# Optimization experiments

Measured on AMD Instinct MI355X. Metric: run time of the kernel, lower is better.

The kernel has to match this reference:

```python
import jax, jax.numpy as jnp
import numpy as np

BLANK = 0
SIZE_AVERAGE = True


def rnnt_loss(acts, labels, act_lens, label_lens):
    # acts: (B, T, U+1, V) raw logits; warp-transducer applies log_softmax internally
    B, T, U1, V = acts.shape
    U = U1 - 1
    logp = jax.nn.log_softmax(acts, axis=-1)          # (B,T,U1,V)
    lp_blank = logp[..., BLANK]                       # (B,T,U1)
    # emission log-prob of label u at grid point (t,u): logp[b,t,u,labels[b,u]]
    lp_emit = jnp.take_along_axis(
        logp[:, :, :U, :], labels[:, None, :, None].astype(jnp.int32), axis=3
    )[..., 0]                                         # (B,T,U)

    # alpha[0,0]=0 ; alpha[0,u] = sum_{k<u} emit[0,k]
    row0 = jnp.concatenate(
        [jnp.zeros((B, 1), acts.dtype), jnp.cumsum(lp_emit[:, 0, :], axis=1)], axis=1
    )                                                 # (B,U1)

    def outer(prev_row, xs):
        blank_prev, emit_t = xs                       # (B,U1), (B,U)
        fb = prev_row + blank_prev                    # arrive via blank from t-1
        def inner(carry, x):
            fb_u, em_prev = x                         # (B,), (B,)
            a = jnp.logaddexp(fb_u, carry + em_prev)  # blank vs emit path
            return a, a
        _, rest = jax.lax.scan(inner, fb[:, 0], (fb[:, 1:].T, emit_t.T))  # (U,B)
        row = jnp.concatenate([fb[:, :1], rest.T], axis=1)               # (B,U1)
        return row, row

    xs = (jnp.moveaxis(lp_blank[:, :-1, :], 1, 0),   # (T-1,B,U1)
          jnp.moveaxis(lp_emit[:, 1:, :], 1, 0))     # (T-1,B,U)
    _, rows = jax.lax.scan(outer, row0, xs)          # (T-1,B,U1)
    alpha = jnp.concatenate([row0[None], rows], axis=0)  # (T,B,U1)

    b_idx = jnp.arange(B)
    t_idx = act_lens.astype(jnp.int32) - 1
    u_idx = label_lens.astype(jnp.int32)
    loglike = alpha[t_idx, b_idx, u_idx] + lp_blank[b_idx, t_idx, u_idx]
    total = -jnp.sum(loglike)
    if SIZE_AVERAGE:
        total = total / B
    return total.reshape(1)


def setup_inputs() -> dict:
    key = jax.random.key(0)
    k1, k2, k3, k4 = jax.random.split(key, 4)
    B, T, U, V = 8, 256, 100, 128
    acts = jax.random.normal(k1, (B, T, U + 1, V), dtype=jnp.float32)
    labels = jax.random.randint(k2, (B, U), 0, V, dtype=jnp.int64)
    act_lens = jax.random.randint(k3, (B,), T // 2, T + 1, dtype=jnp.int32)
    label_lens = jax.random.randint(k4, (B,), U // 2, U + 1, dtype=jnp.int32)
    return {"acts": acts, "labels": labels, "act_lens": act_lens, "label_lens": label_lens}


def reference(acts, labels, act_lens, label_lens):
    return rnnt_loss(acts, labels, act_lens, label_lens)
```

## Files before the change

### kernel.cpp

```cpp
#include <hip/hip_runtime.h>
#include <math.h>

#define B_DIM  8
#define T_DIM  256
#define U_DIM  100
#define U1_DIM 101
#define V_DIM  128

#define ROWU   128
#define DROWS  360
#define NEGF   (-8.0e29f)
#define LOG2E  1.4426950408889634f
#define LN2    0.69314718055994530942f

#define VROWU  312
#define NITMAX 88
#define LDS_BYTES (NITMAX * VROWU * 4)

typedef unsigned uv2 __attribute__((ext_vector_type(2)));

__device__ __forceinline__ float ubit(unsigned u) { return __builtin_bit_cast(float, u); }

__device__ __forceinline__ float logadd2(float a, float b) {
    float m = fmaxf(a, b);
    float e = exp2f(-fabsf(a - b));
    return m + log2f(1.0f + e);
}
__device__ __forceinline__ float lse3(float a, float b, float c) {
    float m = fmaxf(fmaxf(a, b), c);
    float s = exp2f(a - m) + exp2f(b - m) + exp2f(c - m);
    return m + log2f(s);
}
__device__ __forceinline__ float lse5(float a, float b, float c, float d, float e) {
    float m = fmaxf(fmaxf(fmaxf(a, b), c), fmaxf(d, e));
    float s = exp2f(a - m) + exp2f(b - m) + exp2f(c - m) + exp2f(d - m) + exp2f(e - m);
    return m + log2f(s);
}

__device__ __forceinline__ float lane_shr1(float x) {
    int r = __builtin_amdgcn_update_dpp(0, __builtin_bit_cast(int, x),
                                        0x138 , 0xF, 0xF, true);
    return __builtin_bit_cast(float, r);
}

__device__ __forceinline__ unsigned f2bf(float f) {
    unsigned u = __builtin_bit_cast(unsigned, f);
    u += 0x7FFF + ((u >> 16) & 1);
    return u >> 16;
}

__global__ __launch_bounds__(256) void lsm_kernel(
    const float* __restrict__ acts, const int* __restrict__ labels,
    const int* __restrict__ act_lens, const int* __restrict__ label_lens,
    unsigned short* __restrict__ comb, int* __restrict__ counter, int nrows)
{
    if (blockIdx.x == 0 && threadIdx.x == 0) *counter = 0;

    int rid = blockIdx.x * 8 + (threadIdx.x >> 5);
    if (rid >= nrows) return;
    int hl = threadIdx.x & 31;

    int u  = rid % U1_DIM;
    int bt = rid / U1_DIM;
    int b  = bt / T_DIM;
    int t  = bt - b * T_DIM;
    if (t >= act_lens[b] || u > label_lens[b]) return;

    const float* row = acts + (size_t)rid * V_DIM;
    float4 x = *reinterpret_cast<const float4*>(row + 4 * hl);
    float4 y = make_float4(x.x * LOG2E, x.y * LOG2E, x.z * LOG2E, x.w * LOG2E);

    float s = exp2f(y.x) + exp2f(y.y) + exp2f(y.z) + exp2f(y.w);
    #pragma unroll
    for (int off = 16; off; off >>= 1) s += __shfl_xor(s, off);
    float lse2 = log2f(s);

    unsigned short* C = comb + (size_t)b * DROWS * (ROWU * 2);
    int d = t + u + 1;

    if (hl == 0)
        C[(size_t)d * (ROWU * 2) + 2 * u] = (unsigned short)f2bf(y.x - lse2);
    if (u < U_DIM) {
        int lab = labels[b * U_DIM + u];
        if (hl == (lab >> 2)) {
            int r = lab & 3;
            float v = (r == 0) ? y.x : (r == 1) ? y.y : (r == 2) ? y.z : y.w;
            C[(size_t)d * (ROWU * 2) + 2 * u + 3] = (unsigned short)f2bf(v - lse2);
        }
    }
}

struct W2 { float tA, mA, lA, tB, mB, lB; };
__device__ __forceinline__ W2 buildW2m(uv2 c0, uv2 cm, int l, int d, int tl, int ul) {
    const int ua = 2 * l, ub = 2 * l + 1;
    float BL0a = ubit(c0.x << 16), EM0a = ubit(c0.x & 0xFFFF0000u);
    float BL0b = ubit(c0.y << 16), EM0b = ubit(c0.y & 0xFFFF0000u);
    float BLma = ubit(cm.x << 16), EMma = ubit(cm.x & 0xFFFF0000u);
    float BLmb = ubit(cm.y << 16), EMmb = ubit(cm.y & 0xFFFF0000u);
    BL0a = (ua <= ul && (unsigned)(d - 1 - ua) <= (unsigned)tl) ? BL0a : NEGF;
    BL0b = (ub <= ul && (unsigned)(d - 1 - ub) <= (unsigned)tl) ? BL0b : NEGF;
    EM0a = (ua >= 1 && ua <= ul && (unsigned)(d - ua) <= (unsigned)tl) ? EM0a : NEGF;
    EM0b = (ub <= ul && (unsigned)(d - ub) <= (unsigned)tl) ? EM0b : NEGF;
    BLma = (ua <= ul && (unsigned)(d - 2 - ua) <= (unsigned)tl) ? BLma : NEGF;
    BLmb = (ub <= ul && (unsigned)(d - 1 - ub) <= (unsigned)tl) ? BLmb : NEGF;
    EMma = (ua >= 1 && ua <= ul && (unsigned)(d - 1 - ua) <= (unsigned)tl) ? EMma : NEGF;
    EMmb = (ub <= ul && (unsigned)(d - 1 - ub) <= (unsigned)tl) ? EMmb : NEGF;
    float BLmp = lane_shr1(BLmb), EMmp = lane_shr1(EMmb);
    W2 w;
    w.tA = BLma + BL0a;
    w.mA = logadd2(EMma + BL0a, BLmp + EM0a);
    w.lA = EMmp + EM0a;
    w.tB = BLmb + BL0b;
    w.mB = logadd2(EMmb + BL0b, BLma + EM0b);
    w.lB = EMma + EM0b;
    if (l == 0) { w.mA = NEGF; w.lA = NEGF; w.lB = NEGF; }
    return w;
}

__global__ __launch_bounds__(512, 1) void dp_kernel(
    const unsigned* __restrict__ comb,
    const int* __restrict__ act_lens, const int* __restrict__ label_lens,
    float* __restrict__ loglike, int* __restrict__ counter,
    float* __restrict__ out)
{
    extern __shared__ unsigned sV[];

    const int b = blockIdx.x;
    const int l = threadIdx.x & 63;
    const int w = threadIdx.x >> 6;
    const int tl    = act_lens[b] - 1;
    const int ul    = label_lens[b];
    const int dfin  = tl + ul;
    const int start = dfin & 3;
    const int niter = dfin >> 2;

    const unsigned* combB = comb + (size_t)b * DROWS * ROWU;

    for (int it = w; it < niter; it += 8) {
        const int dt = start + 4 * (it + 1);
        const unsigned* C = combB + (size_t)dt * ROWU + 2 * l;
        uv2 c0 = *(const uv2*)(C);
        uv2 c1 = *(const uv2*)(C - ROWU);
        uv2 c2 = *(const uv2*)(C - 2 * ROWU);
        uv2 c3 = *(const uv2*)(C - 3 * ROWU);

        W2 P = buildW2m(c0, c1, l, dt,     tl, ul);
        W2 Q = buildW2m(c2, c3, l, dt - 2, tl, ul);

        float Qt_b1 = lane_shr1(Q.tB), Qm_b1 = lane_shr1(Q.mB), Ql_b1 = lane_shr1(Q.lB);
        float Qt_a1 = lane_shr1(Q.tA), Qm_a1 = lane_shr1(Q.mA), Ql_a1 = lane_shr1(Q.lA);

        float V0a = P.tA + Q.tA;
        float V1a = logadd2(P.tA + Q.mA, P.mA + Qt_b1);
        float V2a = lse3(P.tA + Q.lA, P.mA + Qm_b1, P.lA + Qt_a1);
        float V3a = logadd2(P.mA + Ql_b1, P.lA + Qm_a1);
        float V4a = P.lA + Ql_a1;
        float V0b = P.tB + Q.tB;
        float V1b = logadd2(P.tB + Q.mB, P.mB + Q.tA);
        float V2b = lse3(P.tB + Q.lB, P.mB + Q.mA, P.lB + Qt_b1);
        float V3b = logadd2(P.mB + Q.lA, P.lB + Qm_b1);
        float V4b = P.lB + Ql_b1;
        if (l == 0) { V1a = NEGF; V2a = NEGF; V3a = NEGF; V4a = NEGF; }

        if (l < 52) {
            unsigned* ro = sV + it * VROWU;
            ro[2 * l]           = f2bf(V0a) | (f2bf(V1a) << 16);
            ro[2 * l + 1]       = f2bf(V0b) | (f2bf(V1b) << 16);
            ro[104 + 2 * l]     = f2bf(V2a) | (f2bf(V3a) << 16);
            ro[104 + 2 * l + 1] = f2bf(V2b) | (f2bf(V3b) << 16);
            ro[208 + 2 * l]     = f2bf(V4a);
            ro[208 + 2 * l + 1] = f2bf(V4b);
        }
    }
    __syncthreads();
    if (w != 0) return;

    float fin_bl = ubit(combB[(size_t)(dfin + 1) * ROWU + ul] << 16);

    float v0 = (l == 0) ? 0.0f : NEGF;
    float v1 = NEGF;
    for (int d = 1; d <= start; ++d) {
        uv2 c = *(const uv2*)(combB + (size_t)d * ROWU + 2 * l);
        const int ua = 2 * l, ub = 2 * l + 1;
        float bl0 = ubit(c.x << 16), em0 = ubit(c.x & 0xFFFF0000u);
        float bl1 = ubit(c.y << 16), em1 = ubit(c.y & 0xFFFF0000u);
        bl0 = (ua <= ul && (unsigned)(d - 1 - ua) <= (unsigned)tl) ? bl0 : NEGF;
        bl1 = (ub <= ul && (unsigned)(d - 1 - ub) <= (unsigned)tl) ? bl1 : NEGF;
        em0 = (ua >= 1 && ua <= ul && (unsigned)(d - ua) <= (unsigned)tl) ? em0 : NEGF;
        em1 = (ub <= ul && (unsigned)(d - ub) <= (unsigned)tl) ? em1 : NEGF;
        float left0 = lane_shr1(v1);
        float a0 = v0 + bl0, p0 = left0 + em0;
        float a1 = v1 + bl1, p1 = v0 + em1;
        v0 = logadd2(a0, p0);
        v1 = logadd2(a1, p1);
    }

    #pragma unroll 4
    for (int it = 0; it < niter; ++it) {
        const unsigned* ro = sV + it * VROWU;
        uv2 a0 = *(const uv2*)(ro + 2 * l);
        uv2 a1 = *(const uv2*)(ro + 104 + 2 * l);
        uv2 a2 = *(const uv2*)(ro + 208 + 2 * l);
        float V0a = ubit(a0.x << 16), V1a = ubit(a0.x & 0xFFFF0000u);
        float V0b = ubit(a0.y << 16), V1b = ubit(a0.y & 0xFFFF0000u);
        float V2a = ubit(a1.x << 16), V3a = ubit(a1.x & 0xFFFF0000u);
        float V2b = ubit(a1.y << 16), V3b = ubit(a1.y & 0xFFFF0000u);
        float V4a = ubit(a2.x << 16), V4b = ubit(a2.y << 16);
        float s1 = lane_shr1(v1);
        float s0 = lane_shr1(v0);
        float s3 = lane_shr1(s1);
        float s2 = lane_shr1(s0);
        float nA = lse5(v0 + V0a, s1 + V1a, s0 + V2a, s3 + V3a, s2 + V4a);
        float nB = lse5(v1 + V0b, v0 + V1b, s1 + V2b, s0 + V3b, s3 + V4b);
        v0 = nA; v1 = nB;
    }

    float res = (ul & 1) ? v1 : v0;
    if (l == (ul >> 1)) {
        loglike[b] = LN2 * (res + fin_bl);
        __threadfence();
        int old = atomicAdd(counter, 1);
        if (old == B_DIM - 1) {
            __threadfence();
            float s = 0.0f;
            #pragma unroll
            for (int i = 0; i < B_DIM; ++i)
                s += __hip_atomic_load(&loglike[i], __ATOMIC_RELAXED,
                                       __HIP_MEMORY_SCOPE_AGENT);
            out[0] = -s / (float)B_DIM;
            __hip_atomic_store(counter, 0, __ATOMIC_RELAXED,
                               __HIP_MEMORY_SCOPE_AGENT);
        }
    }
}

extern "C" void kernel_launch(void* const* d_in, const int* in_sizes, int n_in,
                              void* d_out, int out_size, void* d_ws, size_t ws_size,
                              hipStream_t stream) {
    const float* acts       = (const float*)d_in[0];
    const int*   labels     = (const int*)d_in[1];
    const int*   act_lens   = (const int*)d_in[2];
    const int*   label_lens = (const int*)d_in[3];

    unsigned* comb    = (unsigned*)d_ws;
    float*    loglike = (float*)(comb + (size_t)B_DIM * DROWS * ROWU);
    int*      counter = (int*)(loglike + B_DIM);

    int nrows   = B_DIM * T_DIM * U1_DIM;
    int nblocks = (nrows + 7) / 8;

    hipFuncSetAttribute(reinterpret_cast<const void*>(dp_kernel),
                        hipFuncAttributeMaxDynamicSharedMemorySize, LDS_BYTES);

    lsm_kernel<<<nblocks, 256, 0, stream>>>(acts, labels, act_lens, label_lens,
                                            (unsigned short*)comb, counter, nrows);
    dp_kernel<<<B_DIM, 512, LDS_BYTES, stream>>>(comb, act_lens, label_lens,
                                                 loglike, counter, (float*)d_out);
}
```

Measured before the change: 59.51 us.

## Fuse log-softmax and DP into one persistent kernel with flag-based handoff

Merges the log-softmax producer kernel and the DP kernel into a single launch. Producer blocks write done flags, and the DP blocks spin on them before starting. The precomputed step matrices move from LDS to global memory and are software-prefetched with inline-asm global loads several iterations ahead. The cross-batch reduction now uses per-block flags instead of an atomic counter. This removes one launch gap and the inter-kernel bubble. In exchange it relies on all blocks being co-resident, which risks deadlock or bounded-timeout wrong results. The done flags are never reset, so a later call could read stale MAGIC values as complete.

```diff
diff --git a/kernel.cpp b/kernel.cpp
--- a/kernel.cpp
+++ b/kernel.cpp
@@ -1,5 +1,6 @@
 #include <hip/hip_runtime.h>
 #include <math.h>
+
 
 #define B_DIM  8
 #define T_DIM  256
@@ -13,14 +14,18 @@
 #define LOG2E  1.4426950408889634f
 #define LN2    0.69314718055994530942f
 
-#define VROWU  312
 #define NITMAX 88
-#define LDS_BYTES (NITMAX * VROWU * 4)
+#define VROWU  320
+#define DEPTH  8
+
+#define NPROD  2048
+#define NGRP   12928
+#define MAGICA 0x13579BDF
+#define MAGICB 0x2468ACE1
 
 typedef unsigned uv2 __attribute__((ext_vector_type(2)));
 
 __device__ __forceinline__ float ubit(unsigned u) { return __builtin_bit_cast(float, u); }
-
 __device__ __forceinline__ float logadd2(float a, float b) {
     float m = fmaxf(a, b);
     float e = exp2f(-fabsf(a - b));
@@ -36,58 +41,15 @@
     float s = exp2f(a - m) + exp2f(b - m) + exp2f(c - m) + exp2f(d - m) + exp2f(e - m);
     return m + log2f(s);
 }
-
 __device__ __forceinline__ float lane_shr1(float x) {
     int r = __builtin_amdgcn_update_dpp(0, __builtin_bit_cast(int, x),
                                         0x138 , 0xF, 0xF, true);
     return __builtin_bit_cast(float, r);
 }
-
 __device__ __forceinline__ unsigned f2bf(float f) {
     unsigned u = __builtin_bit_cast(unsigned, f);
     u += 0x7FFF + ((u >> 16) & 1);
     return u >> 16;
-}
-
-__global__ __launch_bounds__(256) void lsm_kernel(
-    const float* __restrict__ acts, const int* __restrict__ labels,
-    const int* __restrict__ act_lens, const int* __restrict__ label_lens,
-    unsigned short* __restrict__ comb, int* __restrict__ counter, int nrows)
-{
-    if (blockIdx.x == 0 && threadIdx.x == 0) *counter = 0;
-
-    int rid = blockIdx.x * 8 + (threadIdx.x >> 5);
-    if (rid >= nrows) return;
-    int hl = threadIdx.x & 31;
-
-    int u  = rid % U1_DIM;
-    int bt = rid / U1_DIM;
-    int b  = bt / T_DIM;
-    int t  = bt - b * T_DIM;
-    if (t >= act_lens[b] || u > label_lens[b]) return;
-
-    const float* row = acts + (size_t)rid * V_DIM;
-    float4 x = *reinterpret_cast<const float4*>(row + 4 * hl);
-    float4 y = make_float4(x.x * LOG2E, x.y * LOG2E, x.z * LOG2E, x.w * LOG2E);
-
-    float s = exp2f(y.x) + exp2f(y.y) + exp2f(y.z) + exp2f(y.w);
-    #pragma unroll
-    for (int off = 16; off; off >>= 1) s += __shfl_xor(s, off);
-    float lse2 = log2f(s);
-
-    unsigned short* C = comb + (size_t)b * DROWS * (ROWU * 2);
-    int d = t + u + 1;
-
-    if (hl == 0)
-        C[(size_t)d * (ROWU * 2) + 2 * u] = (unsigned short)f2bf(y.x - lse2);
-    if (u < U_DIM) {
-        int lab = labels[b * U_DIM + u];
-        if (hl == (lab >> 2)) {
-            int r = lab & 3;
-            float v = (r == 0) ? y.x : (r == 1) ? y.y : (r == 2) ? y.z : y.w;
-            C[(size_t)d * (ROWU * 2) + 2 * u + 3] = (unsigned short)f2bf(v - lse2);
-        }
-    }
 }
 
 struct W2 { float tA, mA, lA, tB, mB, lB; };
@@ -117,68 +79,34 @@
     return w;
 }
 
-__global__ __launch_bounds__(512, 1) void dp_kernel(
-    const unsigned* __restrict__ comb,
-    const int* __restrict__ act_lens, const int* __restrict__ label_lens,
-    float* __restrict__ loglike, int* __restrict__ counter,
-    float* __restrict__ out)
-{
-    extern __shared__ unsigned sV[];
-
-    const int b = blockIdx.x;
-    const int l = threadIdx.x & 63;
-    const int w = threadIdx.x >> 6;
-    const int tl    = act_lens[b] - 1;
-    const int ul    = label_lens[b];
-    const int dfin  = tl + ul;
-    const int start = dfin & 3;
-    const int niter = dfin >> 2;
-
-    const unsigned* combB = comb + (size_t)b * DROWS * ROWU;
-
-    for (int it = w; it < niter; it += 8) {
-        const int dt = start + 4 * (it + 1);
-        const unsigned* C = combB + (size_t)dt * ROWU + 2 * l;
-        uv2 c0 = *(const uv2*)(C);
-        uv2 c1 = *(const uv2*)(C - ROWU);
-        uv2 c2 = *(const uv2*)(C - 2 * ROWU);
-        uv2 c3 = *(const uv2*)(C - 3 * ROWU);
-
-        W2 P = buildW2m(c0, c1, l, dt,     tl, ul);
-        W2 Q = buildW2m(c2, c3, l, dt - 2, tl, ul);
-
-        float Qt_b1 = lane_shr1(Q.tB), Qm_b1 = lane_shr1(Q.mB), Ql_b1 = lane_shr1(Q.lB);
-        float Qt_a1 = lane_shr1(Q.tA), Qm_a1 = lane_shr1(Q.mA), Ql_a1 = lane_shr1(Q.lA);
-
-        float V0a = P.tA + Q.tA;
-        float V1a = logadd2(P.tA + Q.mA, P.mA + Qt_b1);
-        float V2a = lse3(P.tA + Q.lA, P.mA + Qm_b1, P.lA + Qt_a1);
-        float V3a = logadd2(P.mA + Ql_b1, P.lA + Qm_a1);
-        float V4a = P.lA + Ql_a1;
-        float V0b = P.tB + Q.tB;
-        float V1b = logadd2(P.tB + Q.mB, P.mB + Q.tA);
-        float V2b = lse3(P.tB + Q.lB, P.mB + Q.mA, P.lB + Qt_b1);
-        float V3b = logadd2(P.mB + Q.lA, P.lB + Qm_b1);
-        float V4b = P.lB + Ql_b1;
-        if (l == 0) { V1a = NEGF; V2a = NEGF; V3a = NEGF; V4a = NEGF; }
-
-        if (l < 52) {
-            unsigned* ro = sV + it * VROWU;
-            ro[2 * l]           = f2bf(V0a) | (f2bf(V1a) << 16);
-            ro[2 * l + 1]       = f2bf(V0b) | (f2bf(V1b) << 16);
-            ro[104 + 2 * l]     = f2bf(V2a) | (f2bf(V3a) << 16);
-            ro[104 + 2 * l + 1] = f2bf(V2b) | (f2bf(V3b) << 16);
-            ro[208 + 2 * l]     = f2bf(V4a);
-            ro[208 + 2 * l + 1] = f2bf(V4b);
-        }
-    }
-    __syncthreads();
-    if (w != 0) return;
-
-    float fin_bl = ubit(combB[(size_t)(dfin + 1) * ROWU + ul] << 16);
-
-    float v0 = (l == 0) ? 0.0f : NEGF;
-    float v1 = NEGF;
+__device__ __forceinline__ void buildV4(const unsigned* combB, int dt, int l,
+                                        int tl, int ul, float* out) {
+    const unsigned* C = combB + (size_t)dt * ROWU + 2 * l;
+    uv2 c0 = *(const uv2*)(C);
+    uv2 c1 = *(const uv2*)(C - ROWU);
+    uv2 c2 = *(const uv2*)(C - 2 * ROWU);
+    uv2 c3 = *(const uv2*)(C - 3 * ROWU);
+    W2 P = buildW2m(c0, c1, l, dt,     tl, ul);
+    W2 Q = buildW2m(c2, c3, l, dt - 2, tl, ul);
+    float Qt_b1 = lane_shr1(Q.tB), Qm_b1 = lane_shr1(Q.mB), Ql_b1 = lane_shr1(Q.lB);
+    float Qt_a1 = lane_shr1(Q.tA), Qm_a1 = lane_shr1(Q.mA), Ql_a1 = lane_shr1(Q.lA);
+    out[0] = P.tA + Q.tA;
+    out[1] = logadd2(P.tA + Q.mA, P.mA + Qt_b1);
+    out[2] = lse3(P.tA + Q.lA, P.mA + Qm_b1, P.lA + Qt_a1);
+    out[3] = logadd2(P.mA + Ql_b1, P.lA + Qm_a1);
+    out[4] = P.lA + Ql_a1;
+    out[5] = P.tB + Q.tB;
+    out[6] = logadd2(P.tB + Q.mB, P.mB + Q.tA);
+    out[7] = lse3(P.tB + Q.lB, P.mB + Q.mA, P.lB + Qt_b1);
+    out[8] = logadd2(P.mB + Q.lA, P.lB + Qm_b1);
+    out[9] = P.lB + Ql_b1;
+    if (l == 0) { out[1] = NEGF; out[2] = NEGF; out[3] = NEGF; out[4] = NEGF; }
+}
+
+__device__ __forceinline__ void prologue(const unsigned* combB, int start, int l,
+                                         int tl, int ul, float& v0, float& v1) {
+    v0 = (l == 0) ? 0.0f : NEGF;
+    v1 = NEGF;
     for (int d = 1; d <= start; ++d) {
         uv2 c = *(const uv2*)(combB + (size_t)d * ROWU + 2 * l);
         const int ua = 2 * l, ub = 2 * l + 1;
@@ -194,43 +122,178 @@
         v0 = logadd2(a0, p0);
         v1 = logadd2(a1, p1);
     }
-
-    #pragma unroll 4
-    for (int it = 0; it < niter; ++it) {
-        const unsigned* ro = sV + it * VROWU;
-        uv2 a0 = *(const uv2*)(ro + 2 * l);
-        uv2 a1 = *(const uv2*)(ro + 104 + 2 * l);
-        uv2 a2 = *(const uv2*)(ro + 208 + 2 * l);
-        float V0a = ubit(a0.x << 16), V1a = ubit(a0.x & 0xFFFF0000u);
-        float V0b = ubit(a0.y << 16), V1b = ubit(a0.y & 0xFFFF0000u);
-        float V2a = ubit(a1.x << 16), V3a = ubit(a1.x & 0xFFFF0000u);
-        float V2b = ubit(a1.y << 16), V3b = ubit(a1.y & 0xFFFF0000u);
-        float V4a = ubit(a2.x << 16), V4b = ubit(a2.y << 16);
-        float s1 = lane_shr1(v1);
-        float s0 = lane_shr1(v0);
-        float s3 = lane_shr1(s1);
-        float s2 = lane_shr1(s0);
-        float nA = lse5(v0 + V0a, s1 + V1a, s0 + V2a, s3 + V3a, s2 + V4a);
-        float nB = lse5(v1 + V0b, v0 + V1b, s1 + V2b, s0 + V3b, s3 + V4b);
-        v0 = nA; v1 = nB;
-    }
-
-    float res = (ul & 1) ? v1 : v0;
-    if (l == (ul >> 1)) {
-        loglike[b] = LN2 * (res + fin_bl);
-        __threadfence();
-        int old = atomicAdd(counter, 1);
-        if (old == B_DIM - 1) {
+}
+
+__global__ __launch_bounds__(512, 1) void fused_kernel(
+    const float* __restrict__ acts, const int* __restrict__ labels,
+    const int* __restrict__ act_lens, const int* __restrict__ label_lens,
+    unsigned* comb_u, int* done, int* done2, unsigned* V,
+    float* loglike, float* out)
+{
+    if (blockIdx.x >= B_DIM) {
+        const int pb = blockIdx.x - B_DIM;
+        const int hw = threadIdx.x >> 5;
+        const int hl = threadIdx.x & 31;
+        unsigned short* comb = (unsigned short*)comb_u;
+
+        for (int g = pb; g < NGRP; g += NPROD) {
+            int rid = g * 16 + hw;
+            int u  = rid % U1_DIM;
+            int bt = rid / U1_DIM;
+            int b  = bt / T_DIM;
+            int t  = bt - b * T_DIM;
+            if (t >= act_lens[b] || u > label_lens[b]) continue;
+
+            const float* row = acts + (size_t)rid * V_DIM;
+            float4 x = *reinterpret_cast<const float4*>(row + 4 * hl);
+            float4 y = make_float4(x.x * LOG2E, x.y * LOG2E, x.z * LOG2E, x.w * LOG2E);
+            float s = exp2f(y.x) + exp2f(y.y) + exp2f(y.z) + exp2f(y.w);
+            #pragma unroll
+            for (int off = 16; off; off >>= 1) s += __shfl_xor(s, off);
+            float lse2 = log2f(s);
+
+            unsigned short* C = comb + (size_t)b * DROWS * (ROWU * 2);
+            int d = t + u + 1;
+            if (hl == 0)
+                C[(size_t)d * (ROWU * 2) + 2 * u] = (unsigned short)f2bf(y.x - lse2);
+            if (u < U_DIM) {
+                int lab = labels[b * U_DIM + u];
+                if (hl == (lab >> 2)) {
+                    int r = lab & 3;
+                    float v = (r == 0) ? y.x : (r == 1) ? y.y : (r == 2) ? y.z : y.w;
+                    C[(size_t)d * (ROWU * 2) + 2 * u + 3] = (unsigned short)f2bf(v - lse2);
+                }
+            }
+        }
+        __syncthreads();
+        if (threadIdx.x == 0) {
             __threadfence();
-            float s = 0.0f;
+            __hip_atomic_store(&done[pb], (int)MAGICA, __ATOMIC_RELEASE,
+                               __HIP_MEMORY_SCOPE_AGENT);
+        }
+        return;
+    }
+
+    const int b = blockIdx.x;
+    const int l = threadIdx.x & 63;
+    const int w = threadIdx.x >> 6;
+
+    {
+        int tries = 0;
+        for (;;) {
+            int ok = 1;
+            for (int i = threadIdx.x; i < NPROD; i += 512)
+                ok &= (__hip_atomic_load(&done[i], __ATOMIC_ACQUIRE,
+                                         __HIP_MEMORY_SCOPE_AGENT) == (int)MAGICA);
+            if (__syncthreads_and(ok)) break;
+            if (++tries > 4000000) break;
+            __builtin_amdgcn_s_sleep(16);
+        }
+    }
+    __threadfence();
+
+    const unsigned* combB = comb_u + (size_t)b * DROWS * ROWU;
+    const int tl = act_lens[b] - 1;
+    const int ul = label_lens[b];
+    const int dfin  = tl + ul;
+    const int start = dfin & 3;
+    const int niter = dfin >> 2;
+    unsigned* Vb = V + (size_t)b * NITMAX * VROWU;
+
+    for (int it = w; it < niter; it += 8) {
+        int dt = start + 4 * (it + 1);
+        float o[10];
+        buildV4(combB, dt, l, tl, ul, o);
+        if (l < 52) {
+            unsigned* ro = Vb + (size_t)it * VROWU;
+            uv2 p0, p1, p2;
+            p0.x = f2bf(o[0]) | (f2bf(o[1]) << 16); p0.y = f2bf(o[5]) | (f2bf(o[6]) << 16);
+            p1.x = f2bf(o[2]) | (f2bf(o[3]) << 16); p1.y = f2bf(o[7]) | (f2bf(o[8]) << 16);
+            p2.x = f2bf(o[4]);                      p2.y = f2bf(o[9]);
+            *(uv2*)(ro + 2 * l)       = p0;
+            *(uv2*)(ro + 104 + 2 * l) = p1;
+            *(uv2*)(ro + 208 + 2 * l) = p2;
+        }
+    }
+    __syncthreads();
+    if (w != 0) return;
+
+    float fin_bl = ubit(combB[(size_t)(dfin + 1) * ROWU + ul] << 16);
+    float v0, v1;
+    prologue(combB, start, l, tl, ul, v0, v1);
+    float rf0 = NEGF, rf1 = NEGF;
+
+    asm volatile("s_waitcnt vmcnt(0)" ::: "memory");
+
+    const char* Vc = (const char*)Vb + 8 * l;
+    uv2 r0[DEPTH], r1[DEPTH], r2[DEPTH];
+    #pragma unroll
+    for (int j = 0; j < DEPTH; ++j) {
+        const char* p = Vc + (size_t)j * (VROWU * 4);
+        asm volatile("global_load_dwordx2 %0, %1, off" : "=v"(r0[j]) : "v"(p));
+        asm volatile("global_load_dwordx2 %0, %1, off" : "=v"(r1[j]) : "v"(p + 416));
+        asm volatile("global_load_dwordx2 %0, %1, off" : "=v"(r2[j]) : "v"(p + 832));
+    }
+    const int ngroups = (niter + DEPTH - 1) / DEPTH;
+    for (int g = 0; g < ngroups; ++g) {
+        const int it0 = g * DEPTH;
+        #pragma unroll
+        for (int q = 0; q < 2; ++q) {
+            asm volatile("s_waitcnt vmcnt(12)");
+            __builtin_amdgcn_sched_barrier(0);
+            #pragma unroll
+            for (int j4 = 0; j4 < 4; ++j4) {
+                const int J = q * 4 + j4;
+                const int it = it0 + J;
+                uv2 a0 = r0[J], a1 = r1[J], a2 = r2[J];
+                float V0a = ubit(a0.x << 16), V1a = ubit(a0.x & 0xFFFF0000u);
+                float V0b = ubit(a0.y << 16), V1b = ubit(a0.y & 0xFFFF0000u);
+                float V2a = ubit(a1.x << 16), V3a = ubit(a1.x & 0xFFFF0000u);
+                float V2b = ubit(a1.y << 16), V3b = ubit(a1.y & 0xFFFF0000u);
+                float V4a = ubit(a2.x << 16), V4b = ubit(a2.y << 16);
+                float s1 = lane_shr1(v1);
+                float s0 = lane_shr1(v0);
+                float s3 = lane_shr1(s1);
+                float s2 = lane_shr1(s0);
+                float nA = lse5(v0 + V0a, s1 + V1a, s0 + V2a, s3 + V3a, s2 + V4a);
+                float nB = lse5(v1 + V0b, v0 + V1b, s1 + V2b, s0 + V3b, s3 + V4b);
+                if (it == niter - 1) { rf0 = nA; rf1 = nB; }
+                v0 = nA; v1 = nB;
+                int rr = it + DEPTH; rr = rr < NITMAX ? rr : NITMAX - 1;
+                const char* p = Vc + (size_t)rr * (VROWU * 4);
+                asm volatile("global_load_dwordx2 %0, %1, off" : "=v"(r0[J]) : "v"(p));
+                asm volatile("global_load_dwordx2 %0, %1, off" : "=v"(r1[J]) : "v"(p + 416));
+                asm volatile("global_load_dwordx2 %0, %1, off" : "=v"(r2[J]) : "v"(p + 832));
+            }
+        }
+    }
+
+    float res = (ul & 1) ? rf1 : rf0;
+    if (l == (ul >> 1)) loglike[b] = LN2 * (res + fin_bl);
+    __threadfence();
+    if (l == 0)
+        __hip_atomic_store(&done2[b], (int)MAGICB, __ATOMIC_RELEASE,
+                           __HIP_MEMORY_SCOPE_AGENT);
+
+    if (b == 0 && l == 0) {
+        int tries = 0;
+        for (;;) {
+            int ok = 1;
             #pragma unroll
             for (int i = 0; i < B_DIM; ++i)
-                s += __hip_atomic_load(&loglike[i], __ATOMIC_RELAXED,
-                                       __HIP_MEMORY_SCOPE_AGENT);
-            out[0] = -s / (float)B_DIM;
-            __hip_atomic_store(counter, 0, __ATOMIC_RELAXED,
-                               __HIP_MEMORY_SCOPE_AGENT);
-        }
+                ok &= (__hip_atomic_load(&done2[i], __ATOMIC_ACQUIRE,
+                                         __HIP_MEMORY_SCOPE_AGENT) == (int)MAGICB);
+            if (ok) break;
+            if (++tries > 50000000) break;
+            __builtin_amdgcn_s_sleep(16);
+        }
+        __threadfence();
+        float s = 0.0f;
+        #pragma unroll
+        for (int i = 0; i < B_DIM; ++i)
+            s += __hip_atomic_load(&loglike[i], __ATOMIC_RELAXED,
+                                   __HIP_MEMORY_SCOPE_AGENT);
+        out[0] = -s / (float)B_DIM;
     }
 }
 
@@ -243,17 +306,12 @@
     const int*   label_lens = (const int*)d_in[3];
 
     unsigned* comb    = (unsigned*)d_ws;
-    float*    loglike = (float*)(comb + (size_t)B_DIM * DROWS * ROWU);
-    int*      counter = (int*)(loglike + B_DIM);
-
-    int nrows   = B_DIM * T_DIM * U1_DIM;
-    int nblocks = (nrows + 7) / 8;
-
-    hipFuncSetAttribute(reinterpret_cast<const void*>(dp_kernel),
-                        hipFuncAttributeMaxDynamicSharedMemorySize, LDS_BYTES);
-
-    lsm_kernel<<<nblocks, 256, 0, stream>>>(acts, labels, act_lens, label_lens,
-                                            (unsigned short*)comb, counter, nrows);
-    dp_kernel<<<B_DIM, 512, LDS_BYTES, stream>>>(comb, act_lens, label_lens,
-                                                 loglike, counter, (float*)d_out);
-}
+    unsigned* V       = comb + (size_t)B_DIM * DROWS * ROWU;
+    float*    loglike = (float*)(V + (size_t)B_DIM * NITMAX * VROWU);
+    int*      done    = (int*)(loglike + B_DIM);
+    int*      done2   = done + NPROD;
+
+    fused_kernel<<<B_DIM + NPROD, 512, 0, stream>>>(
+        acts, labels, act_lens, label_lens,
+        comb, done, done2, V, loglike, (float*)d_out);
+}
```

Result: slower. 143.2 us (+140.6%).
